# Performance work log

Measured on AMD Instinct MI355X. Metric: run time of the kernel, lower is better.

The kernel has to match this reference:

```python
import jax, jax.numpy as jnp
import numpy as np

B, N, H, FD = 2, 512, 128, 5
NT, SD, L = 3, 4, 3
COPY = 10.0
EPS = 1e-6


def setup_inputs() -> dict:
    key = jax.random.key(0)
    ks = jax.random.split(key, 20)
    node_type = jax.random.randint(ks[0], (B, N, 1), 0, NT).astype(jnp.float32)
    node_state = jax.random.normal(ks[1], (B, N, SD), jnp.float32)
    node_feats = jnp.concatenate([node_type, node_state], axis=-1)  # [B,N,5]
    adj = jax.random.bernoulli(ks[2], 0.05, (B, N, N)).astype(jnp.float32)
    adj = jnp.maximum(adj, adj.transpose(0, 2, 1)) * (1.0 - jnp.eye(N, dtype=jnp.float32))
    scope_node_mask = jax.random.bernoulli(ks[3], 0.5, (B, N)).astype(jnp.float32)
    scope_edge_mask = jax.random.bernoulli(ks[4], 0.5, (B, N, N)).astype(jnp.float32)
    s = 0.02
    p = dict(
        node_feats=node_feats, adj=adj,
        scope_node_mask=scope_node_mask, scope_edge_mask=scope_edge_mask,
        W_in=jax.random.normal(ks[5], (FD, H)) * s, b_in=jnp.zeros((H,)),
        W_mp=jax.random.normal(ks[6], (L, 2 * H, H)) * s, b_mp=jnp.zeros((L, H)),
        Wt1=jax.random.normal(ks[7], (H, H)) * s, bt1=jnp.zeros((H,)),
        Wt2=jax.random.normal(ks[8], (H, NT)) * s, bt2=jnp.zeros((NT,)),
        Ws1=jax.random.normal(ks[9], (H, H)) * s, bs1=jnp.zeros((H,)),
        Ws2=jax.random.normal(ks[10], (H, SD)) * s, bs2=jnp.zeros((SD,)),
        We1=jax.random.normal(ks[11], (4 * H, H)) * s, be1=jnp.zeros((H,)),
        We2=jax.random.normal(ks[12], (H, 3)) * s, be2=jnp.zeros((3,)),
    )
    return p


def _decode_edge_logits(adj, edl, eye):
    probs = jax.nn.softmax(edl, axis=-1)
    p_keep = probs[..., 0]  # EDGE_DELTA_KEEP = 0
    p_add = probs[..., 1]   # EDGE_DELTA_ADD = 1
    cur = (adj > 0.5).astype(edl.dtype)
    p_next = jnp.clip(p_add + p_keep * cur, EPS, 1.0 - EPS)
    el = jnp.log(p_next) - jnp.log1p(-p_next)  # logit
    return jnp.where(eye[None], -1e9, el)


def _forward(node_feats, adj, scope_node_mask, scope_edge_mask,
             W_in, b_in, W_mp, b_mp, Wt1, bt1, Wt2, bt2,
             Ws1, bs1, Ws2, bs2, We1, be1, We2, be2):
    # encoder: input proj + L rounds of [h, adj@h] -> Linear -> ReLU
    h = jax.nn.relu(node_feats @ W_in + b_in)  # [B,N,H]
    for l in range(L):
        msg = jnp.einsum('bij,bjh->bih', adj, h)
        h = jax.nn.relu(jnp.concatenate([h, msg], axis=-1) @ W_mp[l] + b_mp[l])
    # node heads (2-layer MLPs)
    type_local = jax.nn.relu(h @ Wt1 + bt1) @ Wt2 + bt2      # [B,N,NT]
    state_local = jax.nn.relu(h @ Ws1 + bs1) @ Ws2 + bs2     # [B,N,SD]
    # pairwise edge-delta head
    h_i = h[:, :, None, :]
    h_j = h[:, None, :, :]
    pair = jnp.concatenate([
        jnp.broadcast_to(h_i, (B, N, N, H)),
        jnp.broadcast_to(h_j, (B, N, N, H)),
        jnp.abs(h_i - h_j),
        h_i * h_j,
    ], axis=-1)  # [B,N,N,4H]
    edl = jax.nn.relu(pair @ We1 + be1) @ We2 + be2  # [B,N,N,3]
    edl = 0.5 * (edl + edl.transpose(0, 2, 1, 3))
    eye = jnp.eye(N, dtype=bool)
    edl = jnp.where(eye[None, :, :, None], 0.0, edl)
    # merges with copy paths
    cur_type = jnp.clip(node_feats[..., 0].astype(jnp.int32), 0, NT - 1)
    copy_type = jnp.where(jnp.arange(NT) == cur_type[..., None], COPY, -COPY)
    type_full = jnp.where(scope_node_mask[..., None] != 0, type_local, copy_type)
    scope = scope_node_mask[..., None]
    state_full = scope * state_local + (1.0 - scope) * node_feats[..., 1:]
    copy_edl = jnp.broadcast_to(jnp.where(jnp.arange(3) == 0, COPY, -COPY), (B, N, N, 3))
    copy_edl = jnp.where(eye[None, :, :, None], 0.0, copy_edl)
    edl_full = jnp.where(scope_edge_mask[..., None] != 0, edl, copy_edl)
    el_full = _decode_edge_logits(adj, edl_full, eye)
    return type_full, state_full, edl_full, el_full


def reference(node_feats, adj, scope_node_mask, scope_edge_mask,
              W_in, b_in, W_mp, b_mp, Wt1, bt1, Wt2, bt2,
              Ws1, bs1, Ws2, bs2, We1, be1, We2, be2):
    return _forward(node_feats, adj, scope_node_mask, scope_edge_mask,
                    W_in, b_in, W_mp, b_mp, Wt1, bt1, Wt2, bt2,
                    Ws1, bs1, Ws2, bs2, We1, be1, We2, be2)
```

## Files before the change

### kernel.cpp

```cpp
#include <hip/hip_runtime.h>
#include <hip/hip_fp16.h>
#include <math.h>

#define B_ 2
#define N_ 512
#define H_ 128
#define NT_ 3
#define SD_ 4
#define FD_ 5

typedef float f32x4 __attribute__((ext_vector_type(4)));
typedef unsigned int u32x4 __attribute__((ext_vector_type(4)));

#define MFMA4(a0, a1, a2, a3, av, b0, b1, b2, b3) \
    asm("s_nop 1\n\t" \
        "v_mfma_f32_16x16x32_f16 %0, %4, %5, %0\n\t" \
        "v_mfma_f32_16x16x32_f16 %1, %4, %6, %1\n\t" \
        "v_mfma_f32_16x16x32_f16 %2, %4, %7, %2\n\t" \
        "v_mfma_f32_16x16x32_f16 %3, %4, %8, %3" \
        : "+v"(a0), "+v"(a1), "+v"(a2), "+v"(a3) \
        : "v"(av), "v"(b0), "v"(b1), "v"(b2), "v"(b3))

#define MFMA16F(acc, a, b) \
    asm("s_nop 1\n\tv_mfma_f32_16x16x32_f16 %0, %1, %2, %0" \
        : "+v"(acc) : "v"(a), "v"(b))

#define PKMUL(d, a, b) \
    asm("v_pk_mul_f16 %0, %1, %2" : "=v"(d) : "v"(a), "v"(b))
#define PKSUB(d, a, b) \
    asm("v_pk_add_f16 %0, %1, %2 neg_lo:[0,1] neg_hi:[0,1]" \
        : "=v"(d) : "v"(a), "v"(b))
#define CVTPKF16(d, a, b) \
    asm("v_cvt_pkrtz_f16_f32 %0, %1, %2" : "=v"(d) : "v"(a), "v"(b))

static __device__ inline unsigned short f2h(float f) {
    return __half_as_ushort(__float2half(f));
}

__global__ __launch_bounds__(128) void k_input(const float* __restrict__ feats,
                                               const float* __restrict__ W_in,
                                               const float* __restrict__ b_in,
                                               float* __restrict__ hout,
                                               const float* __restrict__ We1,
                                               const float* __restrict__ We2,
                                               unsigned short* __restrict__ wfrag,
                                               unsigned short* __restrict__ wfrag2) {
    int blk = blockIdx.x, tid = threadIdx.x;
    if (blk < B_ * N_) {
        const float* f = feats + (size_t)blk * FD_;
        float acc = b_in[tid];
#pragma unroll
        for (int k = 0; k < FD_; ++k) acc += f[k] * W_in[k * H_ + tid];
        hout[(size_t)blk * H_ + tid] = fmaxf(acc, 0.f);
        return;
    }
    if (blk < B_ * N_ + 32) {
        int t = (blk - B_ * N_) * 128 + tid;
        int lane = t & 63, cg = (t >> 6) & 7, kb = t >> 9;
        int lr = lane & 15, g = lane >> 4;
        int c = cg * 16 + lr;
        unsigned o[4];
#pragma unroll
        for (int p = 0; p < 4; ++p) {
            float a = We1[(size_t)(256 + kb * 32 + 8 * g + 2 * p) * H_ + c];
            float bq = We1[(size_t)(256 + kb * 32 + 8 * g + 2 * p + 1) * H_ + c];
            o[p] = (unsigned)f2h(a) | ((unsigned)f2h(bq) << 16);
        }
        u32x4 v = {o[0], o[1], o[2], o[3]};
        *(u32x4*)(wfrag + (size_t)t * 8) = v;
        return;
    }
    {
        int t = (blk - (B_ * N_ + 32)) * 128 + tid;
        if (t < 256) {
            int kb = t >> 6, lane = t & 63;
            int oc = lane & 15, g = lane >> 4;
            unsigned w[4];
#pragma unroll
            for (int p = 0; p < 4; ++p) {
                int k0 = kb * 32 + g * 8 + 2 * p;
                int k1 = k0 + 1;
                int c0 = ((k0 >> 6) << 6) | ((k0 & 3) << 4) | ((k0 & 63) >> 2);
                int c1 = ((k1 >> 6) << 6) | ((k1 & 3) << 4) | ((k1 & 63) >> 2);
                float v0 = (oc < 3) ? We2[c0 * 3 + oc] : 0.f;
                float v1 = (oc < 3) ? We2[c1 * 3 + oc] : 0.f;
                w[p] = (unsigned)f2h(v0) | ((unsigned)f2h(v1) << 16);
            }
            u32x4 v = {w[0], w[1], w[2], w[3]};
            *(u32x4*)(wfrag2 + (size_t)t * 8) = v;
        }
    }
}

__global__ __launch_bounds__(128) void k_mp(const float* __restrict__ hin,
                                            float* __restrict__ hout,
                                            const float* __restrict__ adj,
                                            const float* __restrict__ Wl,
                                            const float* __restrict__ bl) {
    __shared__ float hi[H_];
    __shared__ float msg[H_];
    __shared__ unsigned short idxs[N_];
    __shared__ float avals[N_];
    __shared__ int cnt2[2];
    int node = blockIdx.x;
    int b = node >> 9;
    int tid = threadIdx.x;
    int w = tid >> 6, lane = tid & 63;
    hi[tid] = hin[(size_t)node * H_ + tid];
    const float* arow = adj + (size_t)node * N_;
    float4 av = ((const float4*)arow)[tid];
    int segbase = w * 256;
    int cum = 0;
#pragma unroll
    for (int q = 0; q < 4; ++q) {
        float a = (&av.x)[q];
        bool pred = (a != 0.f);
        unsigned long long mask = __ballot(pred);
        if (pred) {
            int pos = segbase + cum +
                      (int)__popcll(mask & ((1ull << lane) - 1ull));
            idxs[pos] = (unsigned short)(tid * 4 + q);
            avals[pos] = a;
        }
        cum += (int)__popcll(mask);
    }
    if (lane == 0) cnt2[w] = cum;
    __syncthreads();

    float m = 0.f;
    const float* hb = hin + ((size_t)b * N_) * H_;
    int n0 = cnt2[0], n1 = cnt2[1];
    for (int t = 0; t < n0; ++t)
        m += avals[t] * hb[(size_t)idxs[t] * H_ + tid];
    for (int t = 0; t < n1; ++t)
        m += avals[256 + t] * hb[(size_t)idxs[256 + t] * H_ + tid];
    msg[tid] = m;
    __syncthreads();

    float acc = bl[tid];
#pragma unroll 4
    for (int k = 0; k < H_; ++k) {
        acc += hi[k]  * Wl[(size_t)k * H_ + tid];
        acc += msg[k] * Wl[(size_t)(k + H_) * H_ + tid];
    }
    hout[(size_t)node * H_ + tid] = fmaxf(acc, 0.f);
}

__global__ __launch_bounds__(128) void k_heads(
    const float* __restrict__ h, const float* __restrict__ feats,
    const float* __restrict__ snm,
    const float* __restrict__ Wt1, const float* __restrict__ bt1,
    const float* __restrict__ Wt2, const float* __restrict__ bt2,
    const float* __restrict__ Ws1, const float* __restrict__ bs1,
    const float* __restrict__ Ws2, const float* __restrict__ bs2,
    const float* __restrict__ We1, const float* __restrict__ be1,
    float* __restrict__ Acoef, float* __restrict__ Bcoef,
    unsigned short* __restrict__ hf16,
    float* __restrict__ type_out, float* __restrict__ state_out) {
    __shared__ float hi[H_], hT[H_], hS[H_];
    int node = blockIdx.x, tid = threadIdx.x;
    float hv0 = h[(size_t)node * H_ + tid];
    hi[tid] = hv0;
    hf16[(size_t)node * H_ + tid] = f2h(hv0);
    __syncthreads();
    float at = bt1[tid], as = bs1[tid], aa = be1[tid], ab = 0.f;
#pragma unroll 4
    for (int k = 0; k < H_; ++k) {
        float hv = hi[k];
        at += hv * Wt1[k * H_ + tid];
        as += hv * Ws1[k * H_ + tid];
        aa += hv * We1[k * H_ + tid];
        ab += hv * We1[(k + H_) * H_ + tid];
    }
    hT[tid] = fmaxf(at, 0.f);
    hS[tid] = fmaxf(as, 0.f);
    int c = tid;
    int kp = ((c >> 6) << 6) | ((c & 15) << 2) | ((c >> 4) & 3);
    Acoef[(size_t)node * H_ + kp] = aa;
    Bcoef[(size_t)node * H_ + kp] = ab;
    __syncthreads();
    float sm = snm[node];
    if (tid < NT_) {
        float tl = bt2[tid];
        for (int cc = 0; cc < H_; ++cc) tl += hT[cc] * Wt2[cc * NT_ + tid];
        int ct = (int)feats[(size_t)node * FD_];
        ct = ct < 0 ? 0 : (ct > NT_ - 1 ? NT_ - 1 : ct);
        float cv = (tid == ct) ? 10.f : -10.f;
        type_out[(size_t)node * NT_ + tid] = (sm != 0.f) ? tl : cv;
    }
    if (tid >= 64 && tid < 64 + SD_) {
        int s = tid - 64;
        float sl = bs2[s];
        for (int cc = 0; cc < H_; ++cc) sl += hS[cc] * Ws2[cc * SD_ + s];
        state_out[(size_t)node * SD_ + s] =
            sm * sl + (1.f - sm) * feats[(size_t)node * FD_ + 1 + s];
    }
}

__global__ __launch_bounds__(256, 4) void k_pair2(
    const unsigned short* __restrict__ hf16,
    const float* __restrict__ Acp, const float* __restrict__ Bcp,
    const unsigned short* __restrict__ wfrag,
    const unsigned short* __restrict__ wfrag2,
    const float* __restrict__ be2, const float* __restrict__ sem,
    const float* __restrict__ adj,
    float* __restrict__ edl_out, float* __restrict__ el_out) {

    __shared__ unsigned short tile[2][64][128];

    int bid = blockIdx.x;
    int b = 0, r = bid;
    if (r >= 2304) { b = 1; r -= 2304; }
    int t = 0;
#pragma unroll
    for (int s = 0; s < 7; ++s) {
        int sz = (s + 1) * 64;
        if (r >= sz && t == s) { r -= sz; t = s + 1; }
    }
    int jtile = t, i = r;
    int JT0 = jtile << 6;
    bool diagblk = ((i >> 6) == jtile);
    int bN = b << 9;

    int tid = threadIdx.x;
    int wave = tid >> 6, lane = tid & 63;
    int jh = wave >> 1, ch = wave & 1;
    int lr = lane & 15, g = lane >> 4;

    u32x4 Bf[4][8];
#pragma unroll
    for (int ct = 0; ct < 4; ++ct)
#pragma unroll
        for (int kb = 0; kb < 8; ++kb)
            Bf[ct][kb] = *(const u32x4*)(wfrag +
                (((size_t)kb * 8 + (ch * 4 + ct)) * 64 + lane) * 8);

    const unsigned short* hirow = hf16 + (size_t)(bN + i) * H_;
    u32x4 him[4];
#pragma unroll
    for (int m = 0; m < 4; ++m)
        him[m] = *(const u32x4*)(hirow + 32 * m + 8 * g);

    f32x4 AcoI = *(const f32x4*)(Acp + (size_t)(bN + i) * H_ + ch * 64 + lr * 4);
    f32x4 BcoI = *(const f32x4*)(Bcp + (size_t)(bN + i) * H_ + ch * 64 + lr * 4);

    char* tb0 = (char*)&tile[0][0][0];
    char* tb1 = (char*)&tile[1][0][0];

#pragma unroll
    for (int jt = 0; jt < 2; ++jt) {
        int jloc0 = jh * 32 + jt * 16;
        const unsigned short* hjp =
            hf16 + (size_t)(bN + JT0 + jloc0 + lr) * H_ + 8 * g;
        u32x4 hjall[4];
#pragma unroll
        for (int m = 0; m < 4; ++m)
            hjall[m] = *(const u32x4*)(hjp + 32 * m);
        f32x4 BcJv[4], AcJv[4];
#pragma unroll
        for (int rr = 0; rr < 4; ++rr) {
            size_t jn = (size_t)(bN + JT0 + jloc0 + 4 * g + rr) * H_ +
                        ch * 64 + lr * 4;
            BcJv[rr] = *(const f32x4*)(Bcp + jn);
            AcJv[rr] = *(const f32x4*)(Acp + jn);
        }

        f32x4 acc0 = {0.f,0.f,0.f,0.f}, acc1 = {0.f,0.f,0.f,0.f};
        f32x4 acc2 = {0.f,0.f,0.f,0.f}, acc3 = {0.f,0.f,0.f,0.f};

#pragma unroll
        for (int m = 0; m < 4; ++m) {
            u32x4 tav, uav;
#pragma unroll
            for (int p = 0; p < 4; ++p) {
                unsigned hip_ = him[m][p], hjp_ = hjall[m][p];
                unsigned u_, d_;
                PKMUL(u_, hip_, hjp_);
                PKSUB(d_, hip_, hjp_);
                uav[p] = u_;
                tav[p] = d_ & 0x7fff7fffu;
            }
            MFMA4(acc0, acc1, acc2, acc3, tav,
                  Bf[0][m], Bf[1][m], Bf[2][m], Bf[3][m]);
            MFMA4(acc0, acc1, acc2, acc3, uav,
                  Bf[0][4 + m], Bf[1][4 + m], Bf[2][4 + m], Bf[3][4 + m]);
        }
        asm("s_nop 7\n\ts_nop 7\n\ts_nop 3"
            : "+v"(acc0), "+v"(acc1), "+v"(acc2), "+v"(acc3));

#pragma unroll
        for (int rr = 0; rr < 4; ++rr) {
            int jloc = jloc0 + 4 * g + rr;
            float h10 = fmaxf(acc0[rr] + AcoI[0] + BcJv[rr][0], 0.f);
            float h11 = fmaxf(acc1[rr] + AcoI[1] + BcJv[rr][1], 0.f);
            float h12 = fmaxf(acc2[rr] + AcoI[2] + BcJv[rr][2], 0.f);
            float h13 = fmaxf(acc3[rr] + AcoI[3] + BcJv[rr][3], 0.f);
            float h20 = fmaxf(acc0[rr] + AcJv[rr][0] + BcoI[0], 0.f);
            float h21 = fmaxf(acc1[rr] + AcJv[rr][1] + BcoI[1], 0.f);
            float h22 = fmaxf(acc2[rr] + AcJv[rr][2] + BcoI[2], 0.f);
            float h23 = fmaxf(acc3[rr] + AcJv[rr][3] + BcoI[3], 0.f);
            unsigned w10, w11, w20, w21;
            CVTPKF16(w10, h10, h11); CVTPKF16(w11, h12, h13);
            CVTPKF16(w20, h20, h21); CVTPKF16(w21, h22, h23);
            int byte = jloc * 256 + ch * 128 + lr * 8;
            byte ^= (jloc & 7) << 4;
            uint2 v1; v1.x = w10; v1.y = w11;
            uint2 v2; v2.x = w20; v2.y = w21;
            *(uint2*)(tb0 + byte) = v1;
            *(uint2*)(tb1 + byte) = v2;
        }
    }

    u32x4 Bf2[4];
#pragma unroll
    for (int kb = 0; kb < 4; ++kb)
        Bf2[kb] = *(const u32x4*)(wfrag2 + ((size_t)kb * 64 + lane) * 8);

    __syncthreads();

    f32x4 pacc0 = {0.f,0.f,0.f,0.f}, pacc1 = {0.f,0.f,0.f,0.f};
#pragma unroll
    for (int p = 0; p < 2; ++p) {
        int f = wave + 4 * p;
        int orient = f >> 2, sub = f & 3;
        char* tb = orient ? tb1 : tb0;
        int jloc = sub * 16 + lr;
#pragma unroll
        for (int kb = 0; kb < 4; ++kb) {
            int byte = jloc * 256 + kb * 64 + g * 16;
            byte ^= (jloc & 7) << 4;
            u32x4 a = *(const u32x4*)(tb + byte);
            if (p == 0) { MFMA16F(pacc0, a, Bf2[kb]); }
            else        { MFMA16F(pacc1, a, Bf2[kb]); }
        }
    }
    asm("s_nop 7\n\ts_nop 7\n\ts_nop 3" : "+v"(pacc0), "+v"(pacc1));
    __syncthreads();

    float* sbuf = (float*)&tile[0][0][0];
    if (lr < 3) {
#pragma unroll
        for (int p = 0; p < 2; ++p) {
            int f = wave + 4 * p;
            int orient = f >> 2, sub = f & 3;
            f32x4 pa = p ? pacc1 : pacc0;
#pragma unroll
            for (int rr = 0; rr < 4; ++rr) {
                int jloc = sub * 16 + 4 * g + rr;
                sbuf[((orient << 6) + jloc) * 3 + lr] = pa[rr];
            }
        }
    }
    __syncthreads();

    if (tid < 128) {
        int d = tid & 1, jloc = tid >> 1;
        int jg = JT0 + jloc;
        bool skip = diagblk && (jg < i);
        if (!skip) {
            float s0 = 0.5f * (sbuf[jloc * 3 + 0] + sbuf[(64 + jloc) * 3 + 0]) + be2[0];
            float s1 = 0.5f * (sbuf[jloc * 3 + 1] + sbuf[(64 + jloc) * 3 + 1]) + be2[1];
            float s2 = 0.5f * (sbuf[jloc * 3 + 2] + sbuf[(64 + jloc) * 3 + 2]) + be2[2];
            size_t p = d ? ((size_t)(bN + jg) * N_ + i)
                         : ((size_t)(bN + i) * N_ + jg);
            if (jg == i) {
                edl_out[p * 3 + 0] = 0.f;
                edl_out[p * 3 + 1] = 0.f;
                edl_out[p * 3 + 2] = 0.f;
                el_out[p] = -1e9f;
            } else {
                float msk = sem[p];
                float e0 = (msk != 0.f) ? s0 : 10.f;
                float e1 = (msk != 0.f) ? s1 : -10.f;
                float e2 = (msk != 0.f) ? s2 : -10.f;
                edl_out[p * 3 + 0] = e0;
                edl_out[p * 3 + 1] = e1;
                edl_out[p * 3 + 2] = e2;
                float a = adj[p];
                float cur = (a > 0.5f) ? 1.f : 0.f;
                float mx = fmaxf(e0, fmaxf(e1, e2));
                float x0 = expf(e0 - mx), x1 = expf(e1 - mx), x2 = expf(e2 - mx);
                float inv = 1.f / (x0 + x1 + x2);
                float pn = x1 * inv + x0 * inv * cur;
                pn = fminf(fmaxf(pn, 1e-6f), 1.f - 1e-6f);
                el_out[p] = logf(pn) - log1pf(-pn);
            }
        }
    }
}

extern "C" void kernel_launch(void* const* d_in, const int* in_sizes, int n_in,
                              void* d_out, int out_size, void* d_ws,
                              size_t ws_size, hipStream_t stream) {
    const float* feats = (const float*)d_in[0];
    const float* adj   = (const float*)d_in[1];
    const float* snm   = (const float*)d_in[2];
    const float* sem   = (const float*)d_in[3];
    const float* W_in  = (const float*)d_in[4];
    const float* b_in  = (const float*)d_in[5];
    const float* W_mp  = (const float*)d_in[6];
    const float* b_mp  = (const float*)d_in[7];
    const float* Wt1 = (const float*)d_in[8],  *bt1 = (const float*)d_in[9];
    const float* Wt2 = (const float*)d_in[10], *bt2 = (const float*)d_in[11];
    const float* Ws1 = (const float*)d_in[12], *bs1 = (const float*)d_in[13];
    const float* Ws2 = (const float*)d_in[14], *bs2 = (const float*)d_in[15];
    const float* We1 = (const float*)d_in[16], *be1 = (const float*)d_in[17];
    const float* We2 = (const float*)d_in[18], *be2 = (const float*)d_in[19];

    float* out = (float*)d_out;
    float* type_out  = out;
    float* state_out = out + 3072;
    float* edl_out   = out + 7168;
    float* el_out    = out + 7168 + 1572864;

    float* ws = (float*)d_ws;
    float* hA = ws;
    float* hB = ws + 131072;
    float* Bcp = ws + 262144;
    unsigned short* hf16   = (unsigned short*)(ws + 393216);
    unsigned short* wfrag  = (unsigned short*)(ws + 458752);
    unsigned short* wfrag2 = (unsigned short*)(ws + 475136);
    float* Acp = hA;

    k_input<<<B_ * N_ + 34, 128, 0, stream>>>(feats, W_in, b_in, hA,
                                              We1, We2, wfrag, wfrag2);
    k_mp<<<B_ * N_, H_, 0, stream>>>(hA, hB, adj,
                                     W_mp + 0 * 2 * H_ * H_, b_mp + 0 * H_);
    k_mp<<<B_ * N_, H_, 0, stream>>>(hB, hA, adj,
                                     W_mp + 1 * 2 * H_ * H_, b_mp + 1 * H_);
    k_mp<<<B_ * N_, H_, 0, stream>>>(hA, hB, adj,
                                     W_mp + 2 * 2 * H_ * H_, b_mp + 2 * H_);
    k_heads<<<B_ * N_, H_, 0, stream>>>(hB, feats, snm, Wt1, bt1, Wt2, bt2,
                                        Ws1, bs1, Ws2, bs2, We1, be1,
                                        Acp, Bcp, hf16, type_out, state_out);
    k_pair2<<<4608, 256, 0, stream>>>(hf16, Acp, Bcp, wfrag, wfrag2,
                                      be2, sem, adj, edl_out, el_out);
}
```

Before: 131.2 us.

## Widen pair tiles to 128 columns and move symmetric scatter into transpose kernel

The pair kernel now handles 128-column j tiles per block and writes only the upper-triangle row-major edge logits with coalesced stores. The scattered strided transposed writes and the final decode move into a new 16x16 tiled transpose kernel that mirrors values through shared memory and applies the masks and the logit decode. The goal is to remove uncoalesced stores and reduce block count. The cost is an extra launch, a round trip of edl through global memory, and lower occupancy from the larger LDS tile.

```diff
diff --git a/kernel.cpp b/kernel.cpp
--- a/kernel.cpp
+++ b/kernel.cpp
@@ -197,29 +197,25 @@
     }
 }
 
-__global__ __launch_bounds__(256, 4) void k_pair2(
+__global__ __launch_bounds__(256, 2) void k_pair2(
     const unsigned short* __restrict__ hf16,
     const float* __restrict__ Acp, const float* __restrict__ Bcp,
     const unsigned short* __restrict__ wfrag,
     const unsigned short* __restrict__ wfrag2,
-    const float* __restrict__ be2, const float* __restrict__ sem,
-    const float* __restrict__ adj,
-    float* __restrict__ edl_out, float* __restrict__ el_out) {
-
-    __shared__ unsigned short tile[2][64][128];
+    const float* __restrict__ be2,
+    float* __restrict__ edl_out) {
+
+    __shared__ unsigned short tile[2][128][128];
 
     int bid = blockIdx.x;
     int b = 0, r = bid;
-    if (r >= 2304) { b = 1; r -= 2304; }
-    int t = 0;
-#pragma unroll
-    for (int s = 0; s < 7; ++s) {
-        int sz = (s + 1) * 64;
-        if (r >= sz && t == s) { r -= sz; t = s + 1; }
-    }
-    int jtile = t, i = r;
-    int JT0 = jtile << 6;
-    bool diagblk = ((i >> 6) == jtile);
+    if (r >= 1280) { b = 1; r -= 1280; }
+    int jtile, i;
+    if (r < 128)      { jtile = 0; i = r; }
+    else if (r < 384) { jtile = 1; i = r - 128; }
+    else if (r < 768) { jtile = 2; i = r - 384; }
+    else              { jtile = 3; i = r - 768; }
+    int JT0 = jtile << 7;
     int bN = b << 9;
 
     int tid = threadIdx.x;
@@ -248,8 +244,8 @@
     char* tb1 = (char*)&tile[1][0][0];
 
 #pragma unroll
-    for (int jt = 0; jt < 2; ++jt) {
-        int jloc0 = jh * 32 + jt * 16;
+    for (int jt = 0; jt < 4; ++jt) {
+        int jloc0 = jh * 64 + jt * 16;
         const unsigned short* hjp =
             hf16 + (size_t)(bN + JT0 + jloc0 + lr) * H_ + 8 * g;
         u32x4 hjall[4];
@@ -319,10 +315,11 @@
     __syncthreads();
 
     f32x4 pacc0 = {0.f,0.f,0.f,0.f}, pacc1 = {0.f,0.f,0.f,0.f};
-#pragma unroll
-    for (int p = 0; p < 2; ++p) {
+    f32x4 pacc2 = {0.f,0.f,0.f,0.f}, pacc3 = {0.f,0.f,0.f,0.f};
+#pragma unroll
+    for (int p = 0; p < 4; ++p) {
         int f = wave + 4 * p;
-        int orient = f >> 2, sub = f & 3;
+        int orient = f >> 3, sub = f & 7;
         char* tb = orient ? tb1 : tb0;
         int jloc = sub * 16 + lr;
 #pragma unroll
@@ -330,61 +327,103 @@
             int byte = jloc * 256 + kb * 64 + g * 16;
             byte ^= (jloc & 7) << 4;
             u32x4 a = *(const u32x4*)(tb + byte);
-            if (p == 0) { MFMA16F(pacc0, a, Bf2[kb]); }
-            else        { MFMA16F(pacc1, a, Bf2[kb]); }
-        }
-    }
-    asm("s_nop 7\n\ts_nop 7\n\ts_nop 3" : "+v"(pacc0), "+v"(pacc1));
+            if (p == 0)      { MFMA16F(pacc0, a, Bf2[kb]); }
+            else if (p == 1) { MFMA16F(pacc1, a, Bf2[kb]); }
+            else if (p == 2) { MFMA16F(pacc2, a, Bf2[kb]); }
+            else             { MFMA16F(pacc3, a, Bf2[kb]); }
+        }
+    }
+    asm("s_nop 7\n\ts_nop 7\n\ts_nop 3"
+        : "+v"(pacc0), "+v"(pacc1), "+v"(pacc2), "+v"(pacc3));
     __syncthreads();
 
     float* sbuf = (float*)&tile[0][0][0];
     if (lr < 3) {
 #pragma unroll
-        for (int p = 0; p < 2; ++p) {
+        for (int p = 0; p < 4; ++p) {
             int f = wave + 4 * p;
-            int orient = f >> 2, sub = f & 3;
-            f32x4 pa = p ? pacc1 : pacc0;
+            int orient = f >> 3, sub = f & 7;
+            f32x4 pa = (p == 0) ? pacc0 : (p == 1) ? pacc1
+                     : (p == 2) ? pacc2 : pacc3;
 #pragma unroll
             for (int rr = 0; rr < 4; ++rr) {
                 int jloc = sub * 16 + 4 * g + rr;
-                sbuf[((orient << 6) + jloc) * 3 + lr] = pa[rr];
+                sbuf[((orient << 7) + jloc) * 3 + lr] = pa[rr];
             }
         }
     }
     __syncthreads();
 
-    if (tid < 128) {
-        int d = tid & 1, jloc = tid >> 1;
-        int jg = JT0 + jloc;
-        bool skip = diagblk && (jg < i);
-        if (!skip) {
-            float s0 = 0.5f * (sbuf[jloc * 3 + 0] + sbuf[(64 + jloc) * 3 + 0]) + be2[0];
-            float s1 = 0.5f * (sbuf[jloc * 3 + 1] + sbuf[(64 + jloc) * 3 + 1]) + be2[1];
-            float s2 = 0.5f * (sbuf[jloc * 3 + 2] + sbuf[(64 + jloc) * 3 + 2]) + be2[2];
-            size_t p = d ? ((size_t)(bN + jg) * N_ + i)
-                         : ((size_t)(bN + i) * N_ + jg);
-            if (jg == i) {
-                edl_out[p * 3 + 0] = 0.f;
-                edl_out[p * 3 + 1] = 0.f;
-                edl_out[p * 3 + 2] = 0.f;
-                el_out[p] = -1e9f;
-            } else {
-                float msk = sem[p];
-                float e0 = (msk != 0.f) ? s0 : 10.f;
-                float e1 = (msk != 0.f) ? s1 : -10.f;
-                float e2 = (msk != 0.f) ? s2 : -10.f;
-                edl_out[p * 3 + 0] = e0;
-                edl_out[p * 3 + 1] = e1;
-                edl_out[p * 3 + 2] = e2;
-                float a = adj[p];
-                float cur = (a > 0.5f) ? 1.f : 0.f;
-                float mx = fmaxf(e0, fmaxf(e1, e2));
-                float x0 = expf(e0 - mx), x1 = expf(e1 - mx), x2 = expf(e2 - mx);
-                float inv = 1.f / (x0 + x1 + x2);
-                float pn = x1 * inv + x0 * inv * cur;
-                pn = fminf(fmaxf(pn, 1e-6f), 1.f - 1e-6f);
-                el_out[p] = logf(pn) - log1pf(-pn);
-            }
+#pragma unroll
+    for (int q = 0; q < 2; ++q) {
+        int idx = q * 256 + tid;
+        if (idx < 384) {
+            int jloc = idx / 3, comp = idx - jloc * 3;
+            float v = 0.5f * (sbuf[jloc * 3 + comp] +
+                              sbuf[(128 + jloc) * 3 + comp]) + be2[comp];
+            edl_out[((size_t)(bN + i) * N_ + (JT0 + jloc)) * 3 + comp] = v;
+        }
+    }
+}
+
+__global__ __launch_bounds__(256) void k_tr(float* __restrict__ edl,
+                                            float* __restrict__ el,
+                                            const float* __restrict__ sem,
+                                            const float* __restrict__ adj) {
+    __shared__ float ss[3][16][17];
+    int tid = threadIdx.x;
+    int r = tid >> 4, c = tid & 15;
+    int bid = blockIdx.x;
+    int b = 0, t = bid;
+    if (t >= 528) { b = 1; t -= 528; }
+    int J = (int)((sqrtf(8.f * (float)t + 1.f) - 1.f) * 0.5f);
+    while ((J + 1) * (J + 2) / 2 <= t) ++J;
+    while (J * (J + 1) / 2 > t) --J;
+    int I = t - J * (J + 1) / 2;
+    int i0 = I * 16, j0 = J * 16;
+    int bN = b << 9;
+
+    {
+        const float* src = edl + ((size_t)(bN + i0 + r) * N_ + (j0 + c)) * 3;
+        ss[0][r][c] = src[0];
+        ss[1][r][c] = src[1];
+        ss[2][r][c] = src[2];
+    }
+    __syncthreads();
+
+    for (int pass = 0; pass < 2; ++pass) {
+        if (pass == 1 && I == J) break;
+        int gi, gj;
+        float s0, s1, s2;
+        if (I == J) {
+            gi = i0 + r; gj = j0 + c;
+            int lo = r <= c ? r : c, hi = r <= c ? c : r;
+            s0 = ss[0][lo][hi]; s1 = ss[1][lo][hi]; s2 = ss[2][lo][hi];
+        } else if (pass == 0) {
+            gi = i0 + r; gj = j0 + c;
+            s0 = ss[0][r][c]; s1 = ss[1][r][c]; s2 = ss[2][r][c];
+        } else {
+            gi = j0 + r; gj = i0 + c;
+            s0 = ss[0][c][r]; s1 = ss[1][c][r]; s2 = ss[2][c][r];
+        }
+        size_t p = (size_t)(bN + gi) * N_ + gj;
+        if (gi == gj) {
+            edl[p * 3 + 0] = 0.f; edl[p * 3 + 1] = 0.f; edl[p * 3 + 2] = 0.f;
+            el[p] = -1e9f;
+        } else {
+            float msk = sem[p];
+            float e0 = (msk != 0.f) ? s0 : 10.f;
+            float e1 = (msk != 0.f) ? s1 : -10.f;
+            float e2 = (msk != 0.f) ? s2 : -10.f;
+            edl[p * 3 + 0] = e0; edl[p * 3 + 1] = e1; edl[p * 3 + 2] = e2;
+            float a = adj[p];
+            float cur = (a > 0.5f) ? 1.f : 0.f;
+            float mx = fmaxf(e0, fmaxf(e1, e2));
+            float x0 = expf(e0 - mx), x1 = expf(e1 - mx), x2 = expf(e2 - mx);
+            float inv = 1.f / (x0 + x1 + x2);
+            float pn = x1 * inv + x0 * inv * cur;
+            pn = fminf(fmaxf(pn, 1e-6f), 1.f - 1e-6f);
+            el[p] = logf(pn) - log1pf(-pn);
         }
     }
 }
@@ -433,6 +472,7 @@
     k_heads<<<B_ * N_, H_, 0, stream>>>(hB, feats, snm, Wt1, bt1, Wt2, bt2,
                                         Ws1, bs1, Ws2, bs2, We1, be1,
                                         Acp, Bcp, hf16, type_out, state_out);
-    k_pair2<<<4608, 256, 0, stream>>>(hf16, Acp, Bcp, wfrag, wfrag2,
-                                      be2, sem, adj, edl_out, el_out);
-}
+    k_pair2<<<2560, 256, 0, stream>>>(hf16, Acp, Bcp, wfrag, wfrag2,
+                                      be2, edl_out);
+    k_tr<<<1056, 256, 0, stream>>>(edl_out, el_out, sem, adj);
+}
```

New measurement: 128.8 us. About the same (-1.9%).
